# Kernel tuning notes

Hardware: AMD Instinct MI355X
Metric: run time of the kernel (lower is better)

## Reference

```python
import jax, jax.numpy as jnp
import numpy as np

B, C, H, W = 32, 2, 224, 224
P = 4096   # mask points per instance
N = 256    # HV_NUM_OF_HYPOTHESES


def setup_inputs() -> dict:
    key = jax.random.key(0)
    k1, k2, k3 = jax.random.split(key, 3)
    uv_img = jax.random.normal(k1, (B, C, H, W), dtype=jnp.float32)
    pts = jax.random.randint(k2, (B, P, 2), 0, H, dtype=jnp.int64 if jax.config.read('jax_enable_x64') else jnp.int32)
    pair_idx = jax.random.randint(k3, (B, N, 2), 0, P, dtype=pts.dtype)
    return {"uv_img": uv_img, "pts": pts, "pair_idx": pair_idx}


def _per_instance(uv, p, pi):
    # uv: [2,H,W], p: [P,2] int, pi: [N,2] int
    pt0 = p[pi[:, 0]]                      # [N,2] (row, col)
    pt1 = p[pi[:, 1]]                      # [N,2]
    # uv values at each sampled point: uv_img[:, row, col] -> [N,2]
    uv0 = uv[:, pt0[:, 0], pt0[:, 1]].T    # [N,2]
    uv1 = uv[:, pt1[:, 0], pt1[:, 1]].T    # [N,2]
    pt0f = pt0.astype(uv.dtype)
    pt1f = pt1.astype(uv.dtype)
    # A = [uv0 | -uv1], B = pt1 - pt0 (2x2 pinverse solve per hypothesis)
    A = jnp.stack([uv0, -uv1], axis=-1)    # [N,2,2]
    Bv = (pt1f - pt0f)[..., None]          # [N,2,1]
    X = jnp.matmul(jnp.linalg.pinv(A), Bv) # [N,2,1]
    Y = X[:, 0, :] * uv0 + pt0f            # [N,2] hypotheses (row, col)
    # hypothesis weights: count of mask points whose uv direction agrees
    pts_uv = uv[:, p[:, 0], p[:, 1]].T     # [P,2]
    a = Y[:, None, :] - p[None, :, :].astype(uv.dtype)      # [N,P,2]
    a = a / jnp.linalg.norm(a, axis=-1, keepdims=True)
    agree = jnp.einsum('npk,pk->np', a, pts_uv) > 0          # [N,P]
    w = jnp.sum(agree, axis=-1).astype(uv.dtype)             # [N]
    weighted_mean = jnp.sum(Y * w[:, None], axis=0) / jnp.sum(w)
    return weighted_mean[::-1]             # pixel_xy = (col, row)


def reference(uv_img, pts, pair_idx):
    # filled_pixel_xy: [B, 2]
    return jax.vmap(_per_instance)(uv_img, pts, pair_idx)
```

## Files before the change

kernel.cpp:

```cpp
#include <hip/hip_runtime.h>
#include <hip/hip_fp16.h>

#define BATCH 32
#define CH    2
#define HH    224
#define WW    224
#define PP    4096
#define NN    256
#define SPLIT 32
#define TILE  (PP / SPLIT)
#define TILE2 (TILE / 2)

struct alignas(16) PtPack { __half2 u, v, nc, pad; };

__global__ __launch_bounds__(256, 4)
void hough_partial(const float* __restrict__ uv,
                   const int* __restrict__ pts,
                   const int* __restrict__ pair,
                   double* __restrict__ part)
{
    const int blk = blockIdx.x;
    const int b = blk / SPLIT;
    const int s = blk % SPLIT;
    const int t = threadIdx.x;

    const float* uvb = uv + (size_t)b * CH * HH * WW;
    const int* ptsb = pts + b * PP * 2;

    __shared__ PtPack tile[TILE2];
    if (t < TILE2) {
        const int p = s * TILE + 2 * t;
        const int4 pp = *(const int4*)(ptsb + p * 2);
        const float u0 = uvb[pp.x * WW + pp.y];
        const float v0 = uvb[HH * WW + pp.x * WW + pp.y];
        const float u1 = uvb[pp.z * WW + pp.w];
        const float v1 = uvb[HH * WW + pp.z * WW + pp.w];
        const float c0 = (float)pp.x * u0 + (float)pp.y * v0;
        const float c1 = (float)pp.z * u1 + (float)pp.w * v1;
        PtPack pk;
        pk.u  = __floats2half2_rn(u0, u1);
        pk.v  = __floats2half2_rn(v0, v1);
        pk.nc = __floats2half2_rn(-c0, -c1);
        pk.pad = __floats2half2_rn(0.0f, 0.0f);
        tile[t] = pk;
    }

    const int2 pr = *(const int2*)(pair + (b * NN + t) * 2);
    const int2 p0 = *(const int2*)(ptsb + pr.x * 2);
    const int2 p1 = *(const int2*)(ptsb + pr.y * 2);
    const int y0 = p0.x, x0 = p0.y;
    const int y1 = p1.x, x1 = p1.y;

    const float u0a = uvb[y0 * WW + x0];
    const float u0b = uvb[HH * WW + y0 * WW + x0];
    const float u1a = uvb[y1 * WW + x1];
    const float u1b = uvb[HH * WW + y1 * WW + x1];

    const double a00 = (double)u0a, a01 = -(double)u1a;
    const double a10 = (double)u0b, a11 = -(double)u1b;
    const double b0 = (double)(y1 - y0), b1 = (double)(x1 - x0);
    const double det = a00 * a11 - a01 * a10;
    const double frob2 = a00 * a00 + a01 * a01 + a10 * a10 + a11 * a11;

    double t0;
    if (fabs(det) > 1e-12 * frob2) {
        t0 = (b0 * a11 - b1 * a01) / det;
    } else if (frob2 > 0.0) {
        t0 = (a00 * b0 + a10 * b1) / frob2;
    } else {
        t0 = 0.0;
    }

    const float yy = (float)(t0 * (double)u0a + (double)y0);
    const float yx = (float)(t0 * (double)u0b + (double)x0);

    const float maxab = fmaxf(fabsf(yy), fabsf(yx));
    const float sc = (maxab > 1024.0f) ? (1024.0f / maxab) : 1.0f;
    const __half2 yy2 = __float2half2_rn(yy * sc);
    const __half2 yx2 = __float2half2_rn(yx * sc);
    const __half2 sc2 = __float2half2_rn(sc);

    __syncthreads();

    unsigned negs = 0u;
    #pragma unroll 4
    for (int j = 0; j < TILE2; ++j) {
        const PtPack q = tile[j];
        __half2 d = __hmul2(yy2, q.u);
        d = __hfma2(yx2, q.v, d);
        d = __hfma2(sc2, q.nc, d);
        unsigned ub;
        __builtin_memcpy(&ub, &d, 4);
        negs += (ub >> 15) & 0x00010001u;
    }
    const int cnt = TILE - (int)(negs & 0xFFFFu) - (int)(negs >> 16);

    double wy = (double)cnt * (double)yy;
    double wx = (double)cnt * (double)yx;
    double ww = (double)cnt;
    #pragma unroll
    for (int off = 32; off > 0; off >>= 1) {
        wy += __shfl_down(wy, off);
        wx += __shfl_down(wx, off);
        ww += __shfl_down(ww, off);
    }

    __shared__ double red[4 * 3];
    const int wid = t >> 6;
    if ((t & 63) == 0) {
        red[wid * 3 + 0] = wy;
        red[wid * 3 + 1] = wx;
        red[wid * 3 + 2] = ww;
    }
    __syncthreads();
    if (t == 0) {
        double* o = part + (size_t)blk * 4;
        o[0] = red[0] + red[3] + red[6] + red[9];
        o[1] = red[1] + red[4] + red[7] + red[10];
        o[2] = red[2] + red[5] + red[8] + red[11];
    }
}

__global__ __launch_bounds__(256)
void hough_final(const double* __restrict__ part, float* __restrict__ out)
{
    const int t = threadIdx.x;
    const int bb = t >> 3;
    const int l8 = t & 7;
    double sy = 0.0, sx = 0.0, sw = 0.0;
    #pragma unroll
    for (int k = l8; k < SPLIT; k += 8) {
        const double* o = part + (size_t)(bb * SPLIT + k) * 4;
        sy += o[0];
        sx += o[1];
        sw += o[2];
    }
    #pragma unroll
    for (int off = 1; off < 8; off <<= 1) {
        sy += __shfl_xor(sy, off);
        sx += __shfl_xor(sx, off);
        sw += __shfl_xor(sw, off);
    }
    if (l8 == 0) {
        out[bb * 2 + 0] = (float)(sx / sw);
        out[bb * 2 + 1] = (float)(sy / sw);
    }
}

extern "C" void kernel_launch(void* const* d_in, const int* in_sizes, int n_in,
                              void* d_out, int out_size, void* d_ws, size_t ws_size,
                              hipStream_t stream)
{
    const float* uv   = (const float*)d_in[0];
    const int*   pts  = (const int*)d_in[1];
    const int*   pair = (const int*)d_in[2];
    float* out = (float*)d_out;
    double* part = (double*)d_ws;

    hough_partial<<<BATCH * SPLIT, 256, 0, stream>>>(uv, pts, pair, part);
    hough_final<<<1, 256, 0, stream>>>(part, out);
}
```

Measured before the change: 22.11 us.

## Hoist per-hypothesis solve into its own kernel and fuse final reduction via last-block atomic

```diff
diff --git a/kernel.cpp b/kernel.cpp
--- a/kernel.cpp
+++ b/kernel.cpp
@@ -11,13 +11,68 @@
 #define TILE  (PP / SPLIT)
 #define TILE2 (TILE / 2)
 
+#define WS_Y_OFF    0
+#define WS_PART_OFF (64 * 1024)
+#define WS_CNT_OFF  (96 * 1024)
+#define WS_NEED     (96 * 1024 + 64)
+
 struct alignas(16) PtPack { __half2 u, v, nc, pad; };
 
+__device__ inline float2 solve_pair(const float* __restrict__ uvb,
+                                    const int* __restrict__ ptsb,
+                                    const int* __restrict__ pairb, int n)
+{
+    const int2 pr = *(const int2*)(pairb + n * 2);
+    const int2 p0 = *(const int2*)(ptsb + pr.x * 2);
+    const int2 p1 = *(const int2*)(ptsb + pr.y * 2);
+    const int y0 = p0.x, x0 = p0.y;
+    const int y1 = p1.x, x1 = p1.y;
+
+    const float u0a = uvb[y0 * WW + x0];
+    const float u0b = uvb[HH * WW + y0 * WW + x0];
+    const float u1a = uvb[y1 * WW + x1];
+    const float u1b = uvb[HH * WW + y1 * WW + x1];
+
+    const double a00 = (double)u0a, a01 = -(double)u1a;
+    const double a10 = (double)u0b, a11 = -(double)u1b;
+    const double b0 = (double)(y1 - y0), b1 = (double)(x1 - x0);
+    const double det = a00 * a11 - a01 * a10;
+    const double frob2 = a00 * a00 + a01 * a01 + a10 * a10 + a11 * a11;
+
+    double t0;
+    if (fabs(det) > 1e-12 * frob2) {
+        t0 = (b0 * a11 - b1 * a01) / det;
+    } else if (frob2 > 0.0) {
+        t0 = (a00 * b0 + a10 * b1) / frob2;
+    } else {
+        t0 = 0.0;
+    }
+    return make_float2((float)(t0 * (double)u0a + (double)y0),
+                       (float)(t0 * (double)u0b + (double)x0));
+}
+
+__global__ __launch_bounds__(256)
+void hough_solve(const float* __restrict__ uv,
+                 const int* __restrict__ pts,
+                 const int* __restrict__ pair,
+                 float2* __restrict__ yv,
+                 unsigned* __restrict__ cnt)
+{
+    const int b = blockIdx.x;
+    const int t = threadIdx.x;
+    const float* uvb = uv + (size_t)b * CH * HH * WW;
+    yv[b * NN + t] = solve_pair(uvb, pts + b * PP * 2, pair + b * NN * 2, t);
+    if (b == 0 && t == 0)
+        __hip_atomic_store(cnt, 0u, __ATOMIC_RELAXED, __HIP_MEMORY_SCOPE_AGENT);
+}
+
 __global__ __launch_bounds__(256, 4)
-void hough_partial(const float* __restrict__ uv,
-                   const int* __restrict__ pts,
-                   const int* __restrict__ pair,
-                   double* __restrict__ part)
+void hough_vote(const float* __restrict__ uv,
+                const int* __restrict__ pts,
+                const float2* __restrict__ yv,
+                double* __restrict__ part,
+                unsigned* __restrict__ cnt,
+                float* __restrict__ out)
 {
     const int blk = blockIdx.x;
     const int b = blk / SPLIT;
@@ -45,35 +100,8 @@
         tile[t] = pk;
     }
 
-    const int2 pr = *(const int2*)(pair + (b * NN + t) * 2);
-    const int2 p0 = *(const int2*)(ptsb + pr.x * 2);
-    const int2 p1 = *(const int2*)(ptsb + pr.y * 2);
-    const int y0 = p0.x, x0 = p0.y;
-    const int y1 = p1.x, x1 = p1.y;
-
-    const float u0a = uvb[y0 * WW + x0];
-    const float u0b = uvb[HH * WW + y0 * WW + x0];
-    const float u1a = uvb[y1 * WW + x1];
-    const float u1b = uvb[HH * WW + y1 * WW + x1];
-
-    const double a00 = (double)u0a, a01 = -(double)u1a;
-    const double a10 = (double)u0b, a11 = -(double)u1b;
-    const double b0 = (double)(y1 - y0), b1 = (double)(x1 - x0);
-    const double det = a00 * a11 - a01 * a10;
-    const double frob2 = a00 * a00 + a01 * a01 + a10 * a10 + a11 * a11;
-
-    double t0;
-    if (fabs(det) > 1e-12 * frob2) {
-        t0 = (b0 * a11 - b1 * a01) / det;
-    } else if (frob2 > 0.0) {
-        t0 = (a00 * b0 + a10 * b1) / frob2;
-    } else {
-        t0 = 0.0;
-    }
-
-    const float yy = (float)(t0 * (double)u0a + (double)y0);
-    const float yx = (float)(t0 * (double)u0b + (double)x0);
-
+    const float2 Yn = yv[b * NN + t];
+    const float yy = Yn.x, yx = Yn.y;
     const float maxab = fmaxf(fabsf(yy), fabsf(yx));
     const float sc = (maxab > 1024.0f) ? (1024.0f / maxab) : 1.0f;
     const __half2 yy2 = __float2half2_rn(yy * sc);
@@ -93,11 +121,11 @@
         __builtin_memcpy(&ub, &d, 4);
         negs += (ub >> 15) & 0x00010001u;
     }
-    const int cnt = TILE - (int)(negs & 0xFFFFu) - (int)(negs >> 16);
-
-    double wy = (double)cnt * (double)yy;
-    double wx = (double)cnt * (double)yx;
-    double ww = (double)cnt;
+    const int cw = TILE - (int)(negs & 0xFFFFu) - (int)(negs >> 16);
+
+    double wy = (double)cw * (double)yy;
+    double wx = (double)cw * (double)yx;
+    double ww = (double)cw;
     #pragma unroll
     for (int off = 32; off > 0; off >>= 1) {
         wy += __shfl_down(wy, off);
@@ -105,6 +133,116 @@
         ww += __shfl_down(ww, off);
     }
 
+    __shared__ double red[4 * 3];
+    __shared__ int lastFlag;
+    const int wid = t >> 6;
+    if ((t & 63) == 0) {
+        red[wid * 3 + 0] = wy;
+        red[wid * 3 + 1] = wx;
+        red[wid * 3 + 2] = ww;
+    }
+    __syncthreads();
+    if (t == 0) {
+        double* o = part + (size_t)blk * 4;
+        o[0] = red[0] + red[3] + red[6] + red[9];
+        o[1] = red[1] + red[4] + red[7] + red[10];
+        o[2] = red[2] + red[5] + red[8] + red[11];
+        __threadfence();
+        const unsigned prev = __hip_atomic_fetch_add(
+            cnt, 1u, __ATOMIC_ACQ_REL, __HIP_MEMORY_SCOPE_AGENT);
+        lastFlag = (prev == (unsigned)(gridDim.x - 1));
+    }
+    __syncthreads();
+
+    if (lastFlag) {
+        __threadfence();
+        const int bb = t >> 3;
+        const int l8 = t & 7;
+        double sy = 0.0, sx = 0.0, sw = 0.0;
+        #pragma unroll
+        for (int k = l8; k < SPLIT; k += 8) {
+            const double* o = part + (size_t)(bb * SPLIT + k) * 4;
+            sy += o[0];
+            sx += o[1];
+            sw += o[2];
+        }
+        #pragma unroll
+        for (int off = 1; off < 8; off <<= 1) {
+            sy += __shfl_xor(sy, off);
+            sx += __shfl_xor(sx, off);
+            sw += __shfl_xor(sw, off);
+        }
+        if (l8 == 0) {
+            out[bb * 2 + 0] = (float)(sx / sw);
+            out[bb * 2 + 1] = (float)(sy / sw);
+        }
+    }
+}
+
+__global__ __launch_bounds__(256, 4)
+void hough_partial_fb(const float* __restrict__ uv,
+                      const int* __restrict__ pts,
+                      const int* __restrict__ pair,
+                      double* __restrict__ part)
+{
+    const int blk = blockIdx.x;
+    const int b = blk / SPLIT;
+    const int s = blk % SPLIT;
+    const int t = threadIdx.x;
+
+    const float* uvb = uv + (size_t)b * CH * HH * WW;
+    const int* ptsb = pts + b * PP * 2;
+
+    __shared__ PtPack tile[TILE2];
+    if (t < TILE2) {
+        const int p = s * TILE + 2 * t;
+        const int4 pp = *(const int4*)(ptsb + p * 2);
+        const float u0 = uvb[pp.x * WW + pp.y];
+        const float v0 = uvb[HH * WW + pp.x * WW + pp.y];
+        const float u1 = uvb[pp.z * WW + pp.w];
+        const float v1 = uvb[HH * WW + pp.z * WW + pp.w];
+        const float c0 = (float)pp.x * u0 + (float)pp.y * v0;
+        const float c1 = (float)pp.z * u1 + (float)pp.w * v1;
+        PtPack pk;
+        pk.u  = __floats2half2_rn(u0, u1);
+        pk.v  = __floats2half2_rn(v0, v1);
+        pk.nc = __floats2half2_rn(-c0, -c1);
+        pk.pad = __floats2half2_rn(0.0f, 0.0f);
+        tile[t] = pk;
+    }
+
+    const float2 Yn = solve_pair(uvb, ptsb, pair + b * NN * 2, t);
+    const float yy = Yn.x, yx = Yn.y;
+    const float maxab = fmaxf(fabsf(yy), fabsf(yx));
+    const float sc = (maxab > 1024.0f) ? (1024.0f / maxab) : 1.0f;
+    const __half2 yy2 = __float2half2_rn(yy * sc);
+    const __half2 yx2 = __float2half2_rn(yx * sc);
+    const __half2 sc2 = __float2half2_rn(sc);
+
+    __syncthreads();
+
+    unsigned negs = 0u;
+    #pragma unroll 4
+    for (int j = 0; j < TILE2; ++j) {
+        const PtPack q = tile[j];
+        __half2 d = __hmul2(yy2, q.u);
+        d = __hfma2(yx2, q.v, d);
+        d = __hfma2(sc2, q.nc, d);
+        unsigned ub;
+        __builtin_memcpy(&ub, &d, 4);
+        negs += (ub >> 15) & 0x00010001u;
+    }
+    const int cw = TILE - (int)(negs & 0xFFFFu) - (int)(negs >> 16);
+
+    double wy = (double)cw * (double)yy;
+    double wx = (double)cw * (double)yx;
+    double ww = (double)cw;
+    #pragma unroll
+    for (int off = 32; off > 0; off >>= 1) {
+        wy += __shfl_down(wy, off);
+        wx += __shfl_down(wx, off);
+        ww += __shfl_down(ww, off);
+    }
     __shared__ double red[4 * 3];
     const int wid = t >> 6;
     if ((t & 63) == 0) {
@@ -122,7 +260,7 @@
 }
 
 __global__ __launch_bounds__(256)
-void hough_final(const double* __restrict__ part, float* __restrict__ out)
+void hough_final_fb(const double* __restrict__ part, float* __restrict__ out)
 {
     const int t = threadIdx.x;
     const int bb = t >> 3;
@@ -155,8 +293,17 @@
     const int*   pts  = (const int*)d_in[1];
     const int*   pair = (const int*)d_in[2];
     float* out = (float*)d_out;
-    double* part = (double*)d_ws;
-
-    hough_partial<<<BATCH * SPLIT, 256, 0, stream>>>(uv, pts, pair, part);
-    hough_final<<<1, 256, 0, stream>>>(part, out);
-}
+    char* ws = (char*)d_ws;
+
+    if (ws_size >= WS_NEED) {
+        float2*   yv   = (float2*)(ws + WS_Y_OFF);
+        double*   part = (double*)(ws + WS_PART_OFF);
+        unsigned* cnt  = (unsigned*)(ws + WS_CNT_OFF);
+        hough_solve<<<BATCH, 256, 0, stream>>>(uv, pts, pair, yv, cnt);
+        hough_vote<<<BATCH * SPLIT, 256, 0, stream>>>(uv, pts, yv, part, cnt, out);
+    } else {
+        double* part = (double*)ws;
+        hough_partial_fb<<<BATCH * SPLIT, 256, 0, stream>>>(uv, pts, pair, part);
+        hough_final_fb<<<1, 256, 0, stream>>>(part, out);
+    }
+}
```

Result: slower. 48.89 us (+121.1%).
